# Optimization experiments

Hardware: AMD Instinct MI355X
Metric: run time of the kernel (lower is better)

Reference implementation:

```python
import jax, jax.numpy as jnp
import numpy as np

FEAT_STRIDE = 16
SCORE_THRESH = 0.7
MAX_OUTPUTS = 50


def setup_inputs() -> dict:
    key = jax.random.key(0)
    k1, k2 = jax.random.split(key)
    B = 4096
    img_width = 16384
    feat_width = img_width // FEAT_STRIDE  # 1024
    pred_cls_logit = jax.random.normal(k1, (B, feat_width), dtype=jnp.float32)
    pred_delta = jax.random.normal(k2, (B, feat_width, 2), dtype=jnp.float32)
    return {"pred_cls_logit": pred_cls_logit, "pred_delta": pred_delta, "img_width": img_width}


def _nms_single(positions, scores):
    # positions: [N,2] float32, scores: [N] float32 (post-sigmoid)
    # TF version gathers entries with score >= thresh; we keep fixed shape with a
    # validity mask (score of invalid entries set to -inf) for jit-compatibility.
    valid = scores >= SCORE_THRESH
    cent = positions.mean(axis=1)                       # [N]
    n = jnp.sum(valid).astype(jnp.float32)
    vmin = jnp.min(jnp.where(valid, cent, jnp.inf))
    vmax = jnp.max(jnp.where(valid, cent, -jnp.inf))
    # note: the original code OVERWRITES the distance_thresh arg with this value
    dthresh = 0.55 * (vmax - vmin) / (n - 1.0)
    neg_inf = jnp.float32(-jnp.inf)
    work = jnp.where(valid, scores, neg_inf)

    def step(work, _):
        idx = jnp.argmax(work)                          # greedy: highest remaining score
        ok = work[idx] > neg_inf                        # any candidate left?
        sel_s = scores[idx]
        sel_p = positions[idx]
        sel_c = cent[idx]
        # TF keeps |dist| > thresh, i.e. suppress |dist| <= thresh (incl. self)
        suppress = jnp.abs(cent - sel_c) <= dthresh
        work = jnp.where(suppress, neg_inf, work)
        out_p = jnp.where(ok, sel_p, 0.0)               # pad_to_fixed_size -> zeros
        out_s = jnp.where(ok, sel_s, 0.0)
        return work, (out_p, out_s)

    _, (nms_pos, nms_sc) = jax.lax.scan(step, work, None, length=MAX_OUTPUTS)
    return nms_pos, nms_sc[:, None]                     # [50,2], [50,1]


def reference(pred_cls_logit, pred_delta, img_width):
    feat_width = pred_delta.shape[1]
    # interval centers, broadcast over the 2-wide position pair
    centers = (jnp.arange(feat_width, dtype=jnp.float32) + 0.5) * FEAT_STRIDE  # [Fw]
    pos = pred_delta * FEAT_STRIDE + centers[None, :, None]                    # [B,Fw,2]
    w = jnp.float32(img_width)
    pos = jnp.clip(pos, 0.0, w - 1.0)
    scores = jax.nn.sigmoid(pred_cls_logit)                                    # [B,Fw]
    nms_positions, nms_scores = jax.vmap(_nms_single)(pos, scores)
    return nms_positions, nms_scores
```

## Files before the change

### kernel.cpp

```cpp
#include <hip/hip_runtime.h>
#include <stdint.h>

typedef unsigned int u32;

#define FW   1024
#define NOUT 50
#define RPB  4
#define CAP  320
#define SPL  5

#define DPP_UMAX_STEP(m, ctrl)                                                 \
  do {                                                                         \
    const u32 _t = (u32)__builtin_amdgcn_update_dpp(0, (int)(m), (ctrl),       \
                                                    0xf, 0xf, false);          \
    (m) = (m) > _t ? (m) : _t;                                                 \
  } while (0)
#define DPP_FMAX_STEP(m, ctrl)                                                 \
  do {                                                                         \
    const float _t = __uint_as_float((u32)__builtin_amdgcn_update_dpp(         \
        __float_as_int(m), __float_as_int(m), (ctrl), 0xf, 0xf, false));       \
    (m) = fmaxf((m), _t);                                                      \
  } while (0)
#define DPP_FMIN_STEP(m, ctrl)                                                 \
  do {                                                                         \
    const float _t = __uint_as_float((u32)__builtin_amdgcn_update_dpp(         \
        __float_as_int(m), __float_as_int(m), (ctrl), 0xf, 0xf, false));       \
    (m) = fminf((m), _t);                                                      \
  } while (0)
#define DPP_SCAN_STEP(x, ctrl, rmask)                                          \
  do {                                                                         \
    const int _t = __builtin_amdgcn_update_dpp(0, (x), (ctrl), (rmask), 0xf,   \
                                               false);                         \
    (x) += _t;                                                                 \
  } while (0)

#define DPP_ALL6(OP, a)                                                        \
  OP(a, 0x111); OP(a, 0x112); OP(a, 0x114); OP(a, 0x118); OP(a, 0x142);        \
  OP(a, 0x143)

__device__ __forceinline__ u32 umax2(u32 a, u32 b) { return a > b ? a : b; }
__device__ __forceinline__ u32 umax3(u32 a, u32 b, u32 c) {
  return umax2(umax2(a, b), c);
}

template <int NS>
__device__ __forceinline__ u32 run_nms(const float2* __restrict__ kc, int nc,
                                       int lane, float dthresh) {
  u32 keys[NS];
  float cents[NS];
  {
    float2 sl[NS];
#pragma unroll
    for (int k = 0; k < NS; ++k) sl[k] = kc[k * 64 + lane];
#pragma unroll
    for (int k = 0; k < NS; ++k) {
      const int q2 = k * 64 + lane;
      keys[k]  = (q2 < nc) ? __float_as_uint(sl[k].x) : 0u;
      cents[k] = sl[k].y;
    }
  }

  u32 acckey = 0;
#pragma unroll
  for (int it = 0; it < NOUT; ++it) {
    u32 m = umax3(keys[0], keys[1], keys[2]);
#pragma unroll
    for (int k = 3; k < NS; ++k) m = umax2(m, keys[k]);
    DPP_UMAX_STEP(m, 0x111);
    DPP_UMAX_STEP(m, 0x112);
    DPP_UMAX_STEP(m, 0x114);
    DPP_UMAX_STEP(m, 0x118);
    DPP_UMAX_STEP(m, 0x142);
    DPP_UMAX_STEP(m, 0x143);
    const u32 best = (u32)__builtin_amdgcn_readlane((int)m, 63);

    const int qs  = 511 - (int)(best & 511u);
    const int qsc = qs < CAP ? qs : CAP - 1;
    const float sel_c = kc[qsc].y;

    acckey = (lane == it) ? best : acckey;

#pragma unroll
    for (int k = 0; k < NS; ++k) {
      keys[k] = (fabsf(cents[k] - sel_c) <= dthresh) ? 0u : keys[k];
    }
  }
  return acckey;
}

__global__ __launch_bounds__(256, 4) void nms1d_kernel(
    const float* __restrict__ logits,
    const float* __restrict__ delta,
    const int* __restrict__ iw_p,
    float* __restrict__ out_pos,
    float* __restrict__ out_sc)
{
  const int wave = threadIdx.x >> 6;
  const int lane = threadIdx.x & 63;
  const int b = blockIdx.x * RPB + wave;

  __shared__ float2 s_kc[RPB][CAP + 1];
  __shared__ float2 s_pp[RPB][CAP + 1];
  float2* __restrict__ kc = s_kc[wave];
  float2* __restrict__ pp = s_pp[wave];

  const float hi = (float)(*iw_p) - 1.0f;

  const float* __restrict__ lrow = logits + (size_t)b * FW;
  const float* __restrict__ drow = delta  + (size_t)b * FW * 2;

  float4 xl0 = *(const float4*)(lrow + lane * 16 + 0);
  float4 xl1 = *(const float4*)(lrow + lane * 16 + 4);
  float4 xl2 = *(const float4*)(lrow + lane * 16 + 8);
  float4 xl3 = *(const float4*)(lrow + lane * 16 + 12);
  float4 dA0 = *(const float4*)(drow + lane * 32 + 0);
  float4 dB0 = *(const float4*)(drow + lane * 32 + 4);
  float4 dA1 = *(const float4*)(drow + lane * 32 + 8);
  float4 dB1 = *(const float4*)(drow + lane * 32 + 12);
  float4 dA2 = *(const float4*)(drow + lane * 32 + 16);
  float4 dB2 = *(const float4*)(drow + lane * 32 + 20);
  float4 dA3 = *(const float4*)(drow + lane * 32 + 24);
  float4 dB3 = *(const float4*)(drow + lane * 32 + 28);

  float sc[16];
  int v = 0;
  const float4 xls[4] = {xl0, xl1, xl2, xl3};
#pragma unroll
  for (int c = 0; c < 4; ++c) {
    const float xs[4] = {xls[c].x, xls[c].y, xls[c].z, xls[c].w};
#pragma unroll
    for (int j = 0; j < 4; ++j) {
      const float s = 1.0f / (1.0f + expf(-xs[j]));
      sc[c * 4 + j] = s;
      v += (s >= 0.7f) ? 1 : 0;
    }
  }

  int incl = v;
  DPP_SCAN_STEP(incl, 0x111, 0xf);
  DPP_SCAN_STEP(incl, 0x112, 0xf);
  DPP_SCAN_STEP(incl, 0x114, 0xf);
  DPP_SCAN_STEP(incl, 0x118, 0xf);
  DPP_SCAN_STEP(incl, 0x142, 0xa);
  DPP_SCAN_STEP(incl, 0x143, 0xc);
  const int base = incl - v;
  const int n = __builtin_amdgcn_readlane(incl, 63);

  float vmin = INFINITY, vmax = -INFINITY;
  int q = base;
  const float4 dAs[4] = {dA0, dA1, dA2, dA3};
  const float4 dBs[4] = {dB0, dB1, dB2, dB3};
#pragma unroll
  for (int c = 0; c < 4; ++c) {
    const float dx[4] = {dAs[c].x, dAs[c].z, dBs[c].x, dBs[c].z};
    const float dy[4] = {dAs[c].y, dAs[c].w, dBs[c].y, dBs[c].w};
#pragma unroll
    for (int j = 0; j < 4; ++j) {
      const int e = c * 4 + j;
      const int f = lane * 16 + e;
      const float center = (float)f * 16.0f + 8.0f;
      float p0 = dx[j] * 16.0f + center;
      float p1 = dy[j] * 16.0f + center;
      p0 = fminf(fmaxf(p0, 0.0f), hi);
      p1 = fminf(fmaxf(p1, 0.0f), hi);
      const float cc = (p0 + p1) * 0.5f;
      const float s = sc[e];
      const bool valid = (s >= 0.7f);
      vmin = valid ? fminf(vmin, cc) : vmin;
      vmax = valid ? fmaxf(vmax, cc) : vmax;
      const int qd = (valid && q < CAP) ? q : CAP;
      const u32 key = ((__float_as_uint(s) - 0x3F333333u) << 9) | (u32)(511 - q);
      kc[qd] = make_float2(__uint_as_float(key), cc);
      pp[qd] = make_float2(p0, p1);
      q += valid ? 1 : 0;
    }
  }

  DPP_ALL6(DPP_FMIN_STEP, vmin);
  DPP_ALL6(DPP_FMAX_STEP, vmax);
  const float dt_part = (0.55f * (vmax - vmin)) / ((float)incl - 1.0f);
  const float dthresh = __uint_as_float(
      (u32)__builtin_amdgcn_readlane(__float_as_int(dt_part), 63));

  const int nc = n < CAP ? n : CAP;
  u32 acckey;
  if (nc <= 256) acckey = run_nms<4>(kc, nc, lane, dthresh);
  else           acckey = run_nms<5>(kc, nc, lane, dthresh);

  if (lane < NOUT) {
    float p0 = 0.0f, p1 = 0.0f, s = 0.0f;
    if (acckey != 0u) {
      const int qw = 511 - (int)(acckey & 511u);
      const float2 sl = pp[qw];
      p0 = sl.x;
      p1 = sl.y;
      s  = __uint_as_float((acckey >> 9) + 0x3F333333u);
    }
    float* __restrict__ orow_p = out_pos + (size_t)b * NOUT * 2;
    float* __restrict__ orow_s = out_sc  + (size_t)b * NOUT;
    *(float2*)(orow_p + lane * 2) = make_float2(p0, p1);
    orow_s[lane] = s;
  }
}

extern "C" void kernel_launch(void* const* d_in, const int* in_sizes, int n_in,
                              void* d_out, int out_size, void* d_ws, size_t ws_size,
                              hipStream_t stream) {
  const float* logits = (const float*)d_in[0];
  const float* delta  = (const float*)d_in[1];
  const int*   iw     = (const int*)d_in[2];
  const int B = in_sizes[0] / FW;
  float* out_pos = (float*)d_out;
  float* out_sc  = (float*)d_out + (size_t)B * NOUT * 2;
  nms1d_kernel<<<(B + RPB - 1) / RPB, RPB * 64, 0, stream>>>(logits, delta, iw, out_pos, out_sc);
}
```

Baseline: 25.69 us.

## Use coalesced interleaved row loads with packed per-group prefix scan

Each lane now reads 2 logits and 2 delta pairs per 128-element group, so consecutive lanes touch consecutive addresses, instead of each lane reading a contiguous 16-element chunk. The goal is better-coalesced global loads. Because each lane's elements are no longer contiguous, the order-preserving compaction needs a prefix count per group: eight 8-bit counts are packed into two words, scanned with DPP, and combined with per-group totals. This adds scan and bit-extraction ALU work in exchange for the more regular memory access.

New measurement: 24.68 us, median of 2. 3.9% less time.

```diff
diff --git a/kernel.cpp b/kernel.cpp
--- a/kernel.cpp
+++ b/kernel.cpp
@@ -109,55 +109,59 @@
   const float* __restrict__ lrow = logits + (size_t)b * FW;
   const float* __restrict__ drow = delta  + (size_t)b * FW * 2;
 
-  float4 xl0 = *(const float4*)(lrow + lane * 16 + 0);
-  float4 xl1 = *(const float4*)(lrow + lane * 16 + 4);
-  float4 xl2 = *(const float4*)(lrow + lane * 16 + 8);
-  float4 xl3 = *(const float4*)(lrow + lane * 16 + 12);
-  float4 dA0 = *(const float4*)(drow + lane * 32 + 0);
-  float4 dB0 = *(const float4*)(drow + lane * 32 + 4);
-  float4 dA1 = *(const float4*)(drow + lane * 32 + 8);
-  float4 dB1 = *(const float4*)(drow + lane * 32 + 12);
-  float4 dA2 = *(const float4*)(drow + lane * 32 + 16);
-  float4 dB2 = *(const float4*)(drow + lane * 32 + 20);
-  float4 dA3 = *(const float4*)(drow + lane * 32 + 24);
-  float4 dB3 = *(const float4*)(drow + lane * 32 + 28);
+  float2 lg[8];
+  float4 dl[8];
+#pragma unroll
+  for (int g = 0; g < 8; ++g)
+    lg[g] = *(const float2*)(lrow + g * 128 + lane * 2);
+#pragma unroll
+  for (int g = 0; g < 8; ++g)
+    dl[g] = *(const float4*)(drow + g * 256 + lane * 4);
 
   float sc[16];
-  int v = 0;
-  const float4 xls[4] = {xl0, xl1, xl2, xl3};
-#pragma unroll
-  for (int c = 0; c < 4; ++c) {
-    const float xs[4] = {xls[c].x, xls[c].y, xls[c].z, xls[c].w};
-#pragma unroll
-    for (int j = 0; j < 4; ++j) {
-      const float s = 1.0f / (1.0f + expf(-xs[j]));
-      sc[c * 4 + j] = s;
-      v += (s >= 0.7f) ? 1 : 0;
-    }
-  }
-
-  int incl = v;
-  DPP_SCAN_STEP(incl, 0x111, 0xf);
-  DPP_SCAN_STEP(incl, 0x112, 0xf);
-  DPP_SCAN_STEP(incl, 0x114, 0xf);
-  DPP_SCAN_STEP(incl, 0x118, 0xf);
-  DPP_SCAN_STEP(incl, 0x142, 0xa);
-  DPP_SCAN_STEP(incl, 0x143, 0xc);
-  const int base = incl - v;
-  const int n = __builtin_amdgcn_readlane(incl, 63);
+  u32 pk0 = 0, pk1 = 0;
+#pragma unroll
+  for (int g = 0; g < 8; ++g) {
+    const float s0 = 1.0f / (1.0f + expf(-lg[g].x));
+    const float s1 = 1.0f / (1.0f + expf(-lg[g].y));
+    sc[2 * g]     = s0;
+    sc[2 * g + 1] = s1;
+    const u32 cnt = (s0 >= 0.7f ? 1u : 0u) + (s1 >= 0.7f ? 1u : 0u);
+    if (g < 4) pk0 += cnt << (8 * g);
+    else       pk1 += cnt << (8 * (g - 4));
+  }
+
+  int i0 = (int)pk0, i1 = (int)pk1;
+  DPP_SCAN_STEP(i0, 0x111, 0xf); DPP_SCAN_STEP(i1, 0x111, 0xf);
+  DPP_SCAN_STEP(i0, 0x112, 0xf); DPP_SCAN_STEP(i1, 0x112, 0xf);
+  DPP_SCAN_STEP(i0, 0x114, 0xf); DPP_SCAN_STEP(i1, 0x114, 0xf);
+  DPP_SCAN_STEP(i0, 0x118, 0xf); DPP_SCAN_STEP(i1, 0x118, 0xf);
+  DPP_SCAN_STEP(i0, 0x142, 0xa); DPP_SCAN_STEP(i1, 0x142, 0xa);
+  DPP_SCAN_STEP(i0, 0x143, 0xc); DPP_SCAN_STEP(i1, 0x143, 0xc);
+  const u32 e0 = (u32)i0 - pk0;
+  const u32 e1 = (u32)i1 - pk1;
+  const u32 t0 = (u32)__builtin_amdgcn_readlane(i0, 63);
+  const u32 t1 = (u32)__builtin_amdgcn_readlane(i1, 63);
+
+  u32 cb[8];
+  u32 run = 0;
+#pragma unroll
+  for (int g = 0; g < 8; ++g) {
+    cb[g] = run;
+    run += ((g < 4 ? t0 : t1) >> (8 * (g & 3))) & 0xFFu;
+  }
+  const int n = (int)run;
 
   float vmin = INFINITY, vmax = -INFINITY;
-  int q = base;
-  const float4 dAs[4] = {dA0, dA1, dA2, dA3};
-  const float4 dBs[4] = {dB0, dB1, dB2, dB3};
-#pragma unroll
-  for (int c = 0; c < 4; ++c) {
-    const float dx[4] = {dAs[c].x, dAs[c].z, dBs[c].x, dBs[c].z};
-    const float dy[4] = {dAs[c].y, dAs[c].w, dBs[c].y, dBs[c].w};
-#pragma unroll
-    for (int j = 0; j < 4; ++j) {
-      const int e = c * 4 + j;
-      const int f = lane * 16 + e;
+#pragma unroll
+  for (int g = 0; g < 8; ++g) {
+    int q = (int)(cb[g] + (((g < 4 ? e0 : e1) >> (8 * (g & 3))) & 0xFFu));
+    const float dx[2] = {dl[g].x, dl[g].z};
+    const float dy[2] = {dl[g].y, dl[g].w};
+#pragma unroll
+    for (int j = 0; j < 2; ++j) {
+      const int e = 2 * g + j;
+      const int f = g * 128 + lane * 2 + j;
       const float center = (float)f * 16.0f + 8.0f;
       float p0 = dx[j] * 16.0f + center;
       float p1 = dy[j] * 16.0f + center;
@@ -178,7 +182,7 @@
 
   DPP_ALL6(DPP_FMIN_STEP, vmin);
   DPP_ALL6(DPP_FMAX_STEP, vmax);
-  const float dt_part = (0.55f * (vmax - vmin)) / ((float)incl - 1.0f);
+  const float dt_part = (0.55f * (vmax - vmin)) / ((float)n - 1.0f);
   const float dthresh = __uint_as_float(
       (u32)__builtin_amdgcn_readlane(__float_as_int(dt_part), 63));
 
```
